# Optimization experiments

Hardware: AMD Instinct MI355X
Metric: run time of the kernel (lower is better)

## Reference

```python
import jax, jax.numpy as jnp
import numpy as np
from jax import lax

B, T, N = 4, 48, 2000
F, H, HEADS, HOR, K = 16, 64, 4, 24, 3
P = H // 2
EPS_BN = 1e-5
EPS_LN = 1e-5
NEG = -1e9


def layer_norm(x, g, b):
    mu = jnp.mean(x, axis=-1, keepdims=True)
    var = jnp.var(x, axis=-1, keepdims=True)
    return (x - mu) * jax.lax.rsqrt(var + EPS_LN) * g + b


def setup_inputs() -> dict:
    key = jax.random.key(0)
    ks = jax.random.split(key, 16)
    s = lambda k, shp, sc: jax.random.normal(k, shp, jnp.float32) * sc
    return {
        "x": s(ks[0], (B, T, N), 1.0),
        "conv_w": s(ks[1], (F, 1, K), 0.3),
        "conv_b": jnp.zeros((F,), jnp.float32),
        "bn_g": jnp.ones((F,), jnp.float32),
        "bn_b": jnp.zeros((F,), jnp.float32),
        "proj_w": s(ks[2], (H, F * T), 0.03),
        "proj_b": jnp.zeros((H,), jnp.float32),
        "ln1_g": jnp.ones((H,), jnp.float32),
        "ln1_b": jnp.zeros((H,), jnp.float32),
        "src_w": s(ks[3], (P, H), 0.1),
        "src_b": jnp.zeros((P,), jnp.float32),
        "dst_w": s(ks[4], (P, H), 0.1),
        "dst_b": jnp.zeros((P,), jnp.float32),
        "edge_scale": jnp.ones((1,), jnp.float32),
        "in_proj_w": s(ks[5], (3 * H, H), 0.1),
        "in_proj_b": jnp.zeros((3 * H,), jnp.float32),
        "out_w": s(ks[6], (H, H), 0.1),
        "out_b": jnp.zeros((H,), jnp.float32),
        "lnA_g": jnp.ones((H,), jnp.float32),
        "lnA_b": jnp.zeros((H,), jnp.float32),
        "pred_w": s(ks[7], (HOR, H), 0.1),
        "pred_b": jnp.zeros((HOR,), jnp.float32),
    }


def reference(x, conv_w, conv_b, bn_g, bn_b, proj_w, proj_b, ln1_g, ln1_b,
              src_w, src_b, dst_w, dst_b, edge_scale,
              in_proj_w, in_proj_b, out_w, out_b, lnA_g, lnA_b,
              pred_w, pred_b):
    # ---- temporal encoding: [B,T,N] -> [B*N,1,T] conv1d(same) ----
    xt = jnp.transpose(x, (0, 2, 1)).reshape(B * N, 1, T)
    h = lax.conv_general_dilated(xt, conv_w, (1,), "SAME",
                                 dimension_numbers=("NCH", "OIH", "NCH"))
    h = h + conv_b[None, :, None]
    # BatchNorm1d in eval mode (running_mean=0, running_var=1)
    h = h * (bn_g * lax.rsqrt(jnp.float32(1.0 + EPS_BN)))[None, :, None] + bn_b[None, :, None]
    h = jax.nn.relu(h)
    # ---- feature projector: flatten [F,T] -> hidden ----
    flat = h.reshape(B * N, F * T)
    z = flat @ proj_w.T + proj_b
    z = jax.nn.relu(layer_norm(z, ln1_g, ln1_b))
    node = z.reshape(B, N, H)
    # ---- dynamic graph generation ----
    src = jax.nn.leaky_relu(node @ src_w.T + src_b, 0.2)  # [B,N,P]
    dst = jax.nn.leaky_relu(node @ dst_w.T + dst_b, 0.2)
    adj = jnp.einsum("bnp,bmp->bnm", src, dst) * edge_scale[0]
    norm = jnp.maximum(jnp.linalg.norm(adj, axis=-1, keepdims=True), 1e-12)
    adj = adj / norm + jnp.eye(N, dtype=adj.dtype)[None]
    neg_mask = jnp.where(adj <= 0, jnp.float32(NEG), jnp.float32(0.0))  # [B,N,N]
    # ---- relational attention (single layer) ----
    residual = node
    qkv = node @ in_proj_w.T + in_proj_b  # [B,N,3H]
    q, k, v = jnp.split(qkv, 3, axis=-1)
    d = H // HEADS
    qh = q.reshape(B, N, HEADS, d)
    kh = k.reshape(B, N, HEADS, d)
    vh = v.reshape(B, N, HEADS, d)
    scores = jnp.einsum("bqhd,bkhd->bhqk", qh, kh) / jnp.sqrt(jnp.float32(d))
    attn = jax.nn.softmax(scores, axis=-1)
    y = jnp.einsum("bhqk,bkhd->bqhd", attn, vh).reshape(B, N, H)
    y = y @ out_w.T + out_b
    # second (adjacency-masked) attention recompute
    w2 = jnp.einsum("bnd,bmd->bnm", y, y) / jnp.sqrt(jnp.float32(H)) + neg_mask
    w2 = jax.nn.softmax(w2, axis=-1)
    y = jnp.einsum("bnm,bmd->bnd", w2, y)
    y = layer_norm(y + residual, lnA_g, lnA_b)
    # ---- horizon predictor ----
    return y @ pred_w.T + pred_b  # [B,N,HOR]
```

## Files before the change

kernel.cpp:

```cpp
#include <hip/hip_runtime.h>
#include <hip/hip_bf16.h>


#define NB 4
#define TT 48
#define NNODES 2000
#define HORZ 24
#define PART_Q 8000

#define D4(a,b) ((a).x*(b).x + (a).y*(b).y + (a).z*(b).z + (a).w*(b).w)
#define FMA4(o,p,v) { (o).x = fmaf((p),(v).x,(o).x); (o).y = fmaf((p),(v).y,(o).y); \
                      (o).z = fmaf((p),(v).z,(o).z); (o).w = fmaf((p),(v).w,(o).w); }

typedef __attribute__((ext_vector_type(8))) short short8;
typedef __attribute__((ext_vector_type(4))) float f32x4;
#define MFMA16(a,b,c) __builtin_amdgcn_mfma_f32_16x16x32_bf16((a),(b),(c),0,0,0)

__device__ __forceinline__ float wsum64(float v) {
#pragma unroll
    for (int m = 1; m < 64; m <<= 1) v += __shfl_xor(v, m, 64);
    return v;
}
__device__ __forceinline__ unsigned short f2bf(float x) {
    unsigned u = __float_as_uint(x);
    unsigned r = (u + 0x7fffu + ((u >> 16) & 1u)) >> 16;
    return (unsigned short)r;
}
__device__ __forceinline__ float bf2f(unsigned short h) {
    return __uint_as_float((unsigned)h << 16);
}

__global__ __launch_bounds__(256) void k_tr(const float* __restrict__ pw,
                                            float* __restrict__ pT) {
    int i = blockIdx.x * 256 + threadIdx.x;
    int h = i / 768, j = i - h * 768;
    pT[((j >> 2) * 64 + h) * 4 + (j & 3)] = pw[i];
}

__global__ __launch_bounds__(64) void k_enc(const float* __restrict__ x,
        const float* __restrict__ cw, const float* __restrict__ cb,
        const float* __restrict__ bg, const float* __restrict__ bb,
        const float* __restrict__ pT, const float* __restrict__ pb,
        const float* __restrict__ g1, const float* __restrict__ b1,
        float* __restrict__ node) {
    __shared__ float xs[8][52];
    __shared__ float hs[8][768];
    __shared__ float wc[16][4];
    int tid = threadIdx.x;
    int g0 = blockIdx.x * 8;

    if (tid < 16) {
        float s = bg[tid] * rsqrtf(1.0f + 1e-5f);
        wc[tid][0] = cw[tid * 3 + 0] * s;
        wc[tid][1] = cw[tid * 3 + 1] * s;
        wc[tid][2] = cw[tid * 3 + 2] * s;
        wc[tid][3] = cb[tid] * s + bb[tid];
    }
    for (int i = tid; i < 8 * TT; i += 64) {
        int m = i & 7, t = i >> 3;
        int g = g0 + m;
        int b = g / NNODES, n = g - b * NNODES;
        xs[m][t + 1] = x[(b * TT + t) * NNODES + n];
    }
    if (tid < 8) { xs[tid][0] = 0.f; xs[tid][TT + 1] = 0.f; }
    __syncthreads();

    for (int m = 0; m < 8; m++) {
        for (int j = tid; j < 16 * TT; j += 64) {
            int f = j / TT, t = j - f * TT;
            float h = wc[f][0] * xs[m][t] + wc[f][1] * xs[m][t + 1] +
                      wc[f][2] * xs[m][t + 2] + wc[f][3];
            hs[m][j] = fmaxf(h, 0.f);
        }
    }
    __syncthreads();

    float acc[8];
    float pbv = pb[tid];
#pragma unroll
    for (int m = 0; m < 8; m++) acc[m] = pbv;
    const float4* pT4v = (const float4*)pT;
    for (int jb = 0; jb < 192; ++jb) {
        float4 wv = pT4v[jb * 64 + tid];
#pragma unroll
        for (int m = 0; m < 8; m++) {
            float4 hv = *(const float4*)&hs[m][jb * 4];
            acc[m] += D4(wv, hv);
        }
    }
    float gg = g1[tid], bbv = b1[tid];
    for (int m = 0; m < 8; m++) {
        float v = acc[m];
        float sm = wsum64(v);
        float sq = wsum64(v * v);
        float mu = sm * (1.f / 64.f);
        float var = sq * (1.f / 64.f) - mu * mu;
        float z = (v - mu) * rsqrtf(var + 1e-5f) * gg + bbv;
        node[(g0 + m) * 64 + tid] = fmaxf(z, 0.f);
    }
}

__global__ __launch_bounds__(256) void k_qkv(const float* __restrict__ node,
        const float* __restrict__ ipw, const float* __restrict__ ipb,
        const float* __restrict__ sw, const float* __restrict__ sb,
        const float* __restrict__ dw, const float* __restrict__ db,
        float* __restrict__ Qb, float* __restrict__ Kb, float* __restrict__ Vb,
        float* __restrict__ Sb, float* __restrict__ Db) {
    __shared__ float nds[8][64];
    int tid = threadIdx.x;
    int g0 = blockIdx.x * 8;
    for (int i = tid; i < 8 * 64; i += 256) {
        nds[i >> 6][i & 63] = node[(size_t)g0 * 64 + i];
    }
    __syncthreads();

    int o = tid;
    const float* wrow; float bias;
    if (o < 192)      { wrow = ipw + o * 64;          bias = ipb[o]; }
    else if (o < 224) { wrow = sw + (o - 192) * 64;   bias = sb[o - 192]; }
    else              { wrow = dw + (o - 224) * 64;   bias = db[o - 224]; }

    float acc[8];
#pragma unroll
    for (int n = 0; n < 8; ++n) acc[n] = bias;

#pragma unroll
    for (int c = 0; c < 4; ++c) {
        const float4* wp = (const float4*)(wrow + c * 16);
        float4 w0 = wp[0], w1 = wp[1], w2 = wp[2], w3 = wp[3];
#pragma unroll
        for (int n = 0; n < 8; ++n) {
            const float4* nr = (const float4*)&nds[n][c * 16];
            float4 a0 = nr[0], a1 = nr[1], a2 = nr[2], a3 = nr[3];
            acc[n] += D4(a0, w0) + D4(a1, w1) + D4(a2, w2) + D4(a3, w3);
        }
    }

    if (o < 64) {
#pragma unroll
        for (int n = 0; n < 8; ++n) Qb[(size_t)(g0 + n) * 64 + o] = acc[n] * 0.25f;
    } else if (o < 128) {
        int oo = o - 64;
#pragma unroll
        for (int n = 0; n < 8; ++n) Kb[(size_t)(g0 + n) * 64 + oo] = acc[n];
    } else if (o < 192) {
        int oo = o - 128;
#pragma unroll
        for (int n = 0; n < 8; ++n) Vb[(size_t)(g0 + n) * 64 + oo] = acc[n];
    } else if (o < 224) {
        int oo = o - 192;
#pragma unroll
        for (int n = 0; n < 8; ++n) {
            float a = acc[n];
            Sb[(size_t)(g0 + n) * 32 + oo] = (a >= 0.f ? a : 0.2f * a);
        }
    } else {
        int oo = o - 224;
#pragma unroll
        for (int n = 0; n < 8; ++n) {
            float a = acc[n];
            Db[(size_t)(g0 + n) * 32 + oo] = (a >= 0.f ? a : 0.2f * a);
        }
    }
}

__global__ __launch_bounds__(256) void k_adj(const float* __restrict__ Sbuf,
        const float* __restrict__ Dbuf, const float* __restrict__ es_p,
        unsigned* __restrict__ maskT, float* __restrict__ ssqP,
        float* __restrict__ adv) {
    __shared__ float Sl[64][32];
    __shared__ float ssqW[4][64];
    int tid = threadIdx.x, bid = blockIdx.x;
    int b = bid >> 7, qt = (bid >> 2) & 31, mc = bid & 3;
    int w = tid >> 6, l = tid & 63;
    int bbase = b * NNODES;
    int qg0 = bbase + qt * 64;
    float es = es_p[0];

    for (int k = 0; k < 2; ++k) {
        int idx = tid + k * 256;
        int row = idx >> 3, cc = idx & 7;
        int qv = qt * 64 + row;
        *(float4*)&Sl[row][cc * 4] =
            *(const float4*)(Sbuf + (size_t)(bbase + min(qv, NNODES - 1)) * 32 + cc * 4);
    }
    __syncthreads();

    float ssqAcc = 0.f;
#pragma unroll
    for (int tt = 0; tt < 2; ++tt) {
        int t = w + tt * 4;
        int mb = mc * 512 + t * 64 + l;
        bool mok = mb < NNODES;
        float4 dr[8];
        const float4* dp = (const float4*)(Dbuf + (size_t)(bbase + (mok ? mb : NNODES - 1)) * 32);
#pragma unroll
        for (int j = 0; j < 8; ++j) dr[j] = dp[j];

        unsigned long long bits = 0ull;
        for (int qq = 0; qq < 64; ++qq) {
            int qv = qt * 64 + qq;
            const float4* sp = (const float4*)&Sl[qq][0];
            float a = 0.f;
#pragma unroll
            for (int j = 0; j < 8; ++j) a += D4(sp[j], dr[j]);
            a *= es;
            if (!mok) a = 0.f;
            bool diag = (mb == qv);
            if (diag && qv < NNODES) adv[qg0 + qq] = a;
            bits |= ((a > 0.f && !diag) ? 1ull : 0ull) << qq;
            float ssqq = wsum64(a * a);
            if (qq == l) ssqAcc += ssqq;
        }
        maskT[((size_t)(b * 64) + qt * 2) * 2048 + mb] = (unsigned)bits;
        maskT[((size_t)(b * 64) + qt * 2 + 1) * 2048 + mb] = (unsigned)(bits >> 32);
    }
    ssqW[w][l] = ssqAcc;
    __syncthreads();
    if (tid < 64) {
        int qv = qt * 64 + tid;
        if (qv < NNODES)
            ssqP[(size_t)mc * PART_Q + qg0 + tid] =
                ssqW[0][tid] + ssqW[1][tid] + ssqW[2][tid] + ssqW[3][tid];
    }
}

__global__ __launch_bounds__(256) void k_diag(const float* __restrict__ ssqP,
        const float* __restrict__ adv, unsigned* __restrict__ maskT) {
    int qg = blockIdx.x * 256 + threadIdx.x;
    if (qg >= PART_Q) return;
    float ss = ssqP[qg] + ssqP[PART_Q + qg] + ssqP[2 * PART_Q + qg] + ssqP[3 * PART_Q + qg];
    float norm = fmaxf(sqrtf(ss), 1e-12f);
    if (adv[qg] > -norm) {
        int b = qg / NNODES, ql = qg - b * NNODES;
        maskT[((size_t)(b * 64) + (ql >> 5)) * 2048 + ql] |= (1u << (ql & 31));
    }
}

__global__ __launch_bounds__(256, 2) void k_a1(const float* __restrict__ Qb,
        const float* __restrict__ Kb, const float* __restrict__ Vb,
        float* __restrict__ Part) {
    __shared__ float Kl[125][64];
    __shared__ float Vl[125][64];
    int tid = threadIdx.x, bid = blockIdx.x;
    int b = bid >> 7, qb = (bid >> 4) & 7, mc = bid & 15;
    int bbase = b * NNODES;
    int w = tid >> 6, l = tid & 63;
    int h = l >> 4, qs = l & 15;
    int qloc0 = qb * 256 + w * 64 + qs;

    for (int k = 0; k < 16; ++k) {
        int idx = tid + k * 256;
        if (idx < 4000) {
            int arr = idx >= 2000 ? 1 : 0;
            int e = arr ? idx - 2000 : idx;
            int r = e >> 4, cc = e & 15;
            int mb = mc * 125 + r;
            float4 v = *(const float4*)((arr ? Vb : Kb) + (size_t)(bbase + mb) * 64 + cc * 4);
            float* dst = arr ? &Vl[0][0] : &Kl[0][0];
            *(float4*)(dst + r * 64 + cc * 4) = v;
        }
    }

    float4 qf[4][4], fo[4][4];
    float sm[4];
#pragma unroll
    for (int qi = 0; qi < 4; ++qi) {
        int qrow = bbase + min(qloc0 + 16 * qi, NNODES - 1);
        const float4* qp = (const float4*)(Qb + (size_t)qrow * 64 + h * 16);
#pragma unroll
        for (int j = 0; j < 4; ++j) {
            qf[qi][j] = qp[j];
            fo[qi][j] = make_float4(0.f, 0.f, 0.f, 0.f);
        }
        sm[qi] = 0.f;
    }
    __syncthreads();

    for (int mi = 0; mi < 125; ++mi) {
        const float4* kr = (const float4*)(&Kl[mi][h * 16]);
        float4 k0 = kr[0], k1 = kr[1], k2 = kr[2], k3 = kr[3];
        float p[4];
#pragma unroll
        for (int qi = 0; qi < 4; ++qi) {
            float s = D4(qf[qi][0], k0) + D4(qf[qi][1], k1) +
                      D4(qf[qi][2], k2) + D4(qf[qi][3], k3);
            p[qi] = __expf(s);
            sm[qi] += p[qi];
        }
        const float4* vr = (const float4*)(&Vl[mi][h * 16]);
        float4 v0 = vr[0], v1 = vr[1], v2 = vr[2], v3 = vr[3];
#pragma unroll
        for (int qi = 0; qi < 4; ++qi) {
            FMA4(fo[qi][0], p[qi], v0) FMA4(fo[qi][1], p[qi], v1)
            FMA4(fo[qi][2], p[qi], v2) FMA4(fo[qi][3], p[qi], v3)
        }
    }

#pragma unroll
    for (int qi = 0; qi < 4; ++qi) {
        int qloc = qloc0 + 16 * qi;
        if (qloc < NNODES) {
            float* base = Part + (size_t)(mc * 68) * PART_Q + bbase + qloc;
#pragma unroll
            for (int j = 0; j < 4; ++j) {
                base[(size_t)(h * 16 + j * 4 + 0) * PART_Q] = fo[qi][j].x;
                base[(size_t)(h * 16 + j * 4 + 1) * PART_Q] = fo[qi][j].y;
                base[(size_t)(h * 16 + j * 4 + 2) * PART_Q] = fo[qi][j].z;
                base[(size_t)(h * 16 + j * 4 + 3) * PART_Q] = fo[qi][j].w;
            }
            base[(size_t)(64 + h) * PART_Q] = sm[qi];
        }
    }
}

__global__ __launch_bounds__(256) void k_a1m(const float* __restrict__ Part,
        const float* __restrict__ ow, const float* __restrict__ ob,
        float* __restrict__ y1) {
    __shared__ float owl[64][64];
    int tid = threadIdx.x;
    for (int i = tid; i < 4096; i += 256) ((float*)owl)[i] = ow[i];
    __syncthreads();
    int qg = blockIdx.x * 256 + tid;
    if (qg >= PART_Q) return;
    float acc[68];
#pragma unroll
    for (int k = 0; k < 68; ++k) acc[k] = 0.f;
    for (int mc = 0; mc < 16; ++mc) {
        const float* p = Part + (size_t)(mc * 68) * PART_Q + qg;
#pragma unroll
        for (int k = 0; k < 68; ++k) acc[k] += p[(size_t)k * PART_Q];
    }
#pragma unroll
    for (int e = 0; e < 64; ++e) acc[e] /= acc[64 + (e >> 4)];
    float* yo = y1 + (size_t)qg * 64;
    for (int d = 0; d < 64; d += 4) {
        float rr[4];
#pragma unroll
        for (int u = 0; u < 4; ++u) {
            float s = ob[d + u];
            const float4* wr = (const float4*)&owl[d + u][0];
#pragma unroll
            for (int e4 = 0; e4 < 16; ++e4) {
                float4 w4 = wr[e4];
                s = fmaf(acc[e4 * 4 + 0], w4.x, s);
                s = fmaf(acc[e4 * 4 + 1], w4.y, s);
                s = fmaf(acc[e4 * 4 + 2], w4.z, s);
                s = fmaf(acc[e4 * 4 + 3], w4.w, s);
            }
            rr[u] = s;
        }
        *(float4*)(yo + d) = make_float4(rr[0], rr[1], rr[2], rr[3]);
    }
}

__global__ __launch_bounds__(256, 2) void k_a2(const float* __restrict__ y1,
        const unsigned* __restrict__ maskTg, float* __restrict__ Part) {
    __shared__ unsigned short Yhi[64 * 72];
    __shared__ unsigned short Ylo[64 * 72];
    __shared__ unsigned short Yt[64 * 72];
    __shared__ unsigned short Pl[4 * 16 * 72];
    __shared__ unsigned maskTl[2 * 256];

    int tid = threadIdx.x, bid = blockIdx.x;
    int b = bid >> 8, qt = (bid >> 3) & 31, mc = bid & 7;
    int wv = tid >> 6, l = tid & 63;
    int l15 = l & 15, lg = l >> 4;
    const float* y1b = y1 + (size_t)(b * NNODES) * 64;

    for (int i = tid; i < 512; i += 256) {
        int wq = i >> 8, ml = i & 255;
        int mg = mc * 256 + ml;
        maskTl[wq * 256 + ml] =
            (mg < NNODES) ? maskTg[((size_t)(b * 64) + qt * 2 + wq) * 2048 + mg] : 0u;
    }

    int qloc_f = min(qt * 64 + wv * 16 + l15, NNODES - 1);
    const float* qrow = y1b + (size_t)qloc_f * 64;
    short8 Ahi0, Ahi1, Alo0, Alo1;
#pragma unroll
    for (int j = 0; j < 8; ++j) {
        float x0 = qrow[lg * 8 + j];
        unsigned short h0 = f2bf(x0);
        Ahi0[j] = (short)h0; Alo0[j] = (short)f2bf(x0 - bf2f(h0));
        float x1 = qrow[32 + lg * 8 + j];
        unsigned short h1 = f2bf(x1);
        Ahi1[j] = (short)h1; Alo1[j] = (short)f2bf(x1 - bf2f(h1));
    }

    f32x4 O0 = {0.f,0.f,0.f,0.f}, O1 = {0.f,0.f,0.f,0.f};
    f32x4 O2 = {0.f,0.f,0.f,0.f}, O3 = {0.f,0.f,0.f,0.f};
    float sumAcc[4] = {0.f, 0.f, 0.f, 0.f};
    int wvbase = wv * 16 * 72;
    int bitb = (wv & 1) * 16 + lg * 4;
    int mword = wv >> 1;

    for (int step = 0; step < 4; ++step) {
        int m0 = mc * 256 + step * 64;
        for (int i = tid; i < 1024; i += 256) {
            int r = i >> 4, c4 = i & 15;
            int mg = m0 + r;
            float4 v = make_float4(0.f, 0.f, 0.f, 0.f);
            if (mg < NNODES) v = *(const float4*)(y1b + (size_t)mg * 64 + c4 * 4);
            unsigned short h0 = f2bf(v.x), h1 = f2bf(v.y), h2 = f2bf(v.z), h3 = f2bf(v.w);
            ushort4 hv = {h0, h1, h2, h3};
            *(ushort4*)&Yhi[r * 72 + c4 * 4] = hv;
            ushort4 lv = {f2bf(v.x - bf2f(h0)), f2bf(v.y - bf2f(h1)),
                          f2bf(v.z - bf2f(h2)), f2bf(v.w - bf2f(h3))};
            *(ushort4*)&Ylo[r * 72 + c4 * 4] = lv;
            Yt[(c4 * 4 + 0) * 72 + r] = h0;
            Yt[(c4 * 4 + 1) * 72 + r] = h1;
            Yt[(c4 * 4 + 2) * 72 + r] = h2;
            Yt[(c4 * 4 + 3) * 72 + r] = h3;
        }
        __syncthreads();

#pragma unroll
        for (int mt = 0; mt < 4; ++mt) {
            int mrow = mt * 16 + l15;
            short8 bh0 = *(const short8*)&Yhi[mrow * 72 + lg * 8];
            short8 bh1 = *(const short8*)&Yhi[mrow * 72 + 32 + lg * 8];
            short8 bl0 = *(const short8*)&Ylo[mrow * 72 + lg * 8];
            short8 bl1 = *(const short8*)&Ylo[mrow * 72 + 32 + lg * 8];
            f32x4 S = {0.f, 0.f, 0.f, 0.f};
            S = MFMA16(Ahi0, bh0, S); S = MFMA16(Ahi1, bh1, S);
            S = MFMA16(Alo0, bh0, S); S = MFMA16(Alo1, bh1, S);
            S = MFMA16(Ahi0, bl0, S); S = MFMA16(Ahi1, bl1, S);
            unsigned mwv = maskTl[mword * 256 + step * 64 + mt * 16 + l15];
#pragma unroll
            for (int r = 0; r < 4; ++r) {
                float p = ((mwv >> (bitb + r)) & 1u) ? __expf(S[r] * 0.125f) : 0.f;
                sumAcc[r] += p;
                Pl[wvbase + (lg * 4 + r) * 72 + mt * 16 + l15] = f2bf(p);
            }
        }

#pragma unroll
        for (int ks = 0; ks < 2; ++ks) {
            short8 pf = *(const short8*)&Pl[wvbase + l15 * 72 + ks * 32 + lg * 8];
            short8 v0 = *(const short8*)&Yt[(0 * 16 + l15) * 72 + ks * 32 + lg * 8];
            O0 = MFMA16(pf, v0, O0);
            short8 v1 = *(const short8*)&Yt[(1 * 16 + l15) * 72 + ks * 32 + lg * 8];
            O1 = MFMA16(pf, v1, O1);
            short8 v2 = *(const short8*)&Yt[(2 * 16 + l15) * 72 + ks * 32 + lg * 8];
            O2 = MFMA16(pf, v2, O2);
            short8 v3 = *(const short8*)&Yt[(3 * 16 + l15) * 72 + ks * 32 + lg * 8];
            O3 = MFMA16(pf, v3, O3);
        }
        __syncthreads();
    }

#pragma unroll
    for (int r = 0; r < 4; ++r) {
        float s = sumAcc[r];
        s += __shfl_xor(s, 1, 64); s += __shfl_xor(s, 2, 64);
        s += __shfl_xor(s, 4, 64); s += __shfl_xor(s, 8, 64);
        sumAcc[r] = s;
    }
    int qrow_base = qt * 64 + wv * 16 + lg * 4;
#pragma unroll
    for (int r = 0; r < 4; ++r) {
        int qloc = qrow_base + r;
        if (qloc < NNODES) {
            float* pp = Part + ((size_t)(mc * 8192) + b * 2048 + qloc) * 72;
            pp[0 * 16 + l15] = O0[r];
            pp[1 * 16 + l15] = O1[r];
            pp[2 * 16 + l15] = O2[r];
            pp[3 * 16 + l15] = O3[r];
            if (l15 == 0) pp[64] = sumAcc[r];
        }
    }
}

__global__ __launch_bounds__(256) void k_a2m(const float* __restrict__ Part,
        const float* __restrict__ node,
        const float* __restrict__ ga, const float* __restrict__ ba,
        const float* __restrict__ pw, const float* __restrict__ pb,
        float* __restrict__ out) {
    __shared__ float pwl[24 * 64];
    __shared__ float gal[64], bal[64], pbl[24];
    int tid = threadIdx.x;
    for (int i = tid; i < 24 * 64; i += 256) pwl[i] = pw[i];
    if (tid < 64) { gal[tid] = ga[tid]; bal[tid] = ba[tid]; }
    if (tid < 24) pbl[tid] = pb[tid];
    __syncthreads();
    int t = blockIdx.x * 256 + tid;
    int b = t >> 11, ql = t & 2047;
    if (ql >= NNODES) return;
    int qg = b * NNODES + ql;

    float acc[65];
#pragma unroll
    for (int k = 0; k < 65; ++k) acc[k] = 0.f;
    for (int mc = 0; mc < 8; ++mc) {
        const float* p = Part + ((size_t)(mc * 8192) + b * 2048 + ql) * 72;
#pragma unroll
        for (int k = 0; k < 65; ++k) acc[k] += p[k];
    }
    float inv = 1.0f / acc[64];
    const float* nd = node + (size_t)qg * 64;
    float oo[64];
    float s1 = 0.f, s2 = 0.f;
#pragma unroll
    for (int d = 0; d < 64; ++d) {
        float v = acc[d] * inv + nd[d];
        oo[d] = v;
        s1 += v; s2 += v * v;
    }
    float mu = s1 * (1.f / 64.f);
    float var = s2 * (1.f / 64.f) - mu * mu;
    float rs = rsqrtf(var + 1e-5f);
#pragma unroll
    for (int d = 0; d < 64; ++d) oo[d] = (oo[d] - mu) * rs * gal[d] + bal[d];

    float* op = out + (size_t)qg * HORZ;
    for (int r = 0; r < HORZ; ++r) {
        float s = pbl[r];
        const float4* wr = (const float4*)&pwl[r * 64];
#pragma unroll
        for (int e4 = 0; e4 < 16; ++e4) {
            float4 w4 = wr[e4];
            s = fmaf(oo[e4 * 4 + 0], w4.x, s);
            s = fmaf(oo[e4 * 4 + 1], w4.y, s);
            s = fmaf(oo[e4 * 4 + 2], w4.z, s);
            s = fmaf(oo[e4 * 4 + 3], w4.w, s);
        }
        op[r] = s;
    }
}

extern "C" void kernel_launch(void* const* d_in, const int* in_sizes, int n_in,
                              void* d_out, int out_size, void* d_ws, size_t ws_size,
                              hipStream_t stream) {
    const float* x      = (const float*)d_in[0];
    const float* conv_w = (const float*)d_in[1];
    const float* conv_b = (const float*)d_in[2];
    const float* bn_g   = (const float*)d_in[3];
    const float* bn_b   = (const float*)d_in[4];
    const float* proj_w = (const float*)d_in[5];
    const float* proj_b = (const float*)d_in[6];
    const float* ln1_g  = (const float*)d_in[7];
    const float* ln1_b  = (const float*)d_in[8];
    const float* src_w  = (const float*)d_in[9];
    const float* src_b  = (const float*)d_in[10];
    const float* dst_w  = (const float*)d_in[11];
    const float* dst_b  = (const float*)d_in[12];
    const float* edge_s = (const float*)d_in[13];
    const float* ipw    = (const float*)d_in[14];
    const float* ipb    = (const float*)d_in[15];
    const float* out_w  = (const float*)d_in[16];
    const float* out_b  = (const float*)d_in[17];
    const float* lnA_g  = (const float*)d_in[18];
    const float* lnA_b  = (const float*)d_in[19];
    const float* pred_w = (const float*)d_in[20];
    const float* pred_b = (const float*)d_in[21];
    float* out = (float*)d_out;

    float* ws = (float*)d_ws;
    float*    projT = ws;
    float*    node  = projT + 49152;
    float*    y1    = node + 512000;
    float*    Qb    = y1 + 512000;
    float*    Kb    = Qb + 512000;
    float*    Vb    = Kb + 512000;
    float*    Sbuf  = Vb + 512000;
    float*    Dbuf  = Sbuf + 256000;
    unsigned* maskT = (unsigned*)(Dbuf + 256000);
    float*    ssqP  = (float*)(maskT + 524288);
    float*    adv   = ssqP + 32000;
    float*    Part  = adv + 8000;

    k_tr<<<192, 256, 0, stream>>>(proj_w, projT);
    k_enc<<<1000, 64, 0, stream>>>(x, conv_w, conv_b, bn_g, bn_b,
                                   projT, proj_b, ln1_g, ln1_b, node);
    k_qkv<<<1000, 256, 0, stream>>>(node, ipw, ipb, src_w, src_b, dst_w, dst_b,
                                    Qb, Kb, Vb, Sbuf, Dbuf);
    k_adj<<<512, 256, 0, stream>>>(Sbuf, Dbuf, edge_s, maskT, ssqP, adv);
    k_diag<<<32, 256, 0, stream>>>(ssqP, adv, maskT);
    k_a1<<<512, 256, 0, stream>>>(Qb, Kb, Vb, Part);
    k_a1m<<<32, 256, 0, stream>>>(Part, out_w, out_b, y1);
    k_a2<<<1024, 256, 0, stream>>>(y1, maskT, Part);
    k_a2m<<<32, 256, 0, stream>>>(Part, node, lnA_g, lnA_b, pred_w, pred_b, out);
}
```

Baseline: 402.8 us.

## Move first attention to bf16 MFMA with split-precision QK and repartition

Rewrites the unmasked multi-head attention kernel to use 16x16x32 bf16 MFMA instructions instead of scalar FP32 dot products. Q and K are split into hi/lo bf16 parts (three-term product) to keep the score precision near FP32, while P and V go through plain bf16 via LDS staging. The grid is repartitioned into 1024 blocks over 64-query tiles and 8 key chunks, and the partial buffer layout becomes row-major per query, with the merge kernel updated to match. The risk is bf16 rounding error in the P*V product and the extra LDS traffic for converting and transposing K/V.

```diff
diff --git a/kernel.cpp b/kernel.cpp
--- a/kernel.cpp
+++ b/kernel.cpp
@@ -9,8 +9,6 @@
 #define PART_Q 8000
 
 #define D4(a,b) ((a).x*(b).x + (a).y*(b).y + (a).z*(b).z + (a).w*(b).w)
-#define FMA4(o,p,v) { (o).x = fmaf((p),(v).x,(o).x); (o).y = fmaf((p),(v).y,(o).y); \
-                      (o).z = fmaf((p),(v).z,(o).z); (o).w = fmaf((p),(v).w,(o).w); }
 
 typedef __attribute__((ext_vector_type(8))) short short8;
 typedef __attribute__((ext_vector_type(4))) float f32x4;
@@ -240,76 +238,121 @@
 __global__ __launch_bounds__(256, 2) void k_a1(const float* __restrict__ Qb,
         const float* __restrict__ Kb, const float* __restrict__ Vb,
         float* __restrict__ Part) {
-    __shared__ float Kl[125][64];
-    __shared__ float Vl[125][64];
+    __shared__ unsigned short Khi[64 * 72];
+    __shared__ unsigned short Klo[64 * 72];
+    __shared__ unsigned short Vt[64 * 73];
+    __shared__ unsigned short Pl[4 * 16 * 72];
+
     int tid = threadIdx.x, bid = blockIdx.x;
-    int b = bid >> 7, qb = (bid >> 4) & 7, mc = bid & 15;
+    int b = bid >> 8, qt = (bid >> 3) & 31, mc = bid & 7;
     int bbase = b * NNODES;
-    int w = tid >> 6, l = tid & 63;
-    int h = l >> 4, qs = l & 15;
-    int qloc0 = qb * 256 + w * 64 + qs;
-
-    for (int k = 0; k < 16; ++k) {
-        int idx = tid + k * 256;
-        if (idx < 4000) {
-            int arr = idx >= 2000 ? 1 : 0;
-            int e = arr ? idx - 2000 : idx;
-            int r = e >> 4, cc = e & 15;
-            int mb = mc * 125 + r;
-            float4 v = *(const float4*)((arr ? Vb : Kb) + (size_t)(bbase + mb) * 64 + cc * 4);
-            float* dst = arr ? &Vl[0][0] : &Kl[0][0];
-            *(float4*)(dst + r * 64 + cc * 4) = v;
-        }
-    }
-
-    float4 qf[4][4], fo[4][4];
-    float sm[4];
-#pragma unroll
-    for (int qi = 0; qi < 4; ++qi) {
-        int qrow = bbase + min(qloc0 + 16 * qi, NNODES - 1);
-        const float4* qp = (const float4*)(Qb + (size_t)qrow * 64 + h * 16);
-#pragma unroll
-        for (int j = 0; j < 4; ++j) {
-            qf[qi][j] = qp[j];
-            fo[qi][j] = make_float4(0.f, 0.f, 0.f, 0.f);
-        }
-        sm[qi] = 0.f;
-    }
-    __syncthreads();
-
-    for (int mi = 0; mi < 125; ++mi) {
-        const float4* kr = (const float4*)(&Kl[mi][h * 16]);
-        float4 k0 = kr[0], k1 = kr[1], k2 = kr[2], k3 = kr[3];
-        float p[4];
-#pragma unroll
-        for (int qi = 0; qi < 4; ++qi) {
-            float s = D4(qf[qi][0], k0) + D4(qf[qi][1], k1) +
-                      D4(qf[qi][2], k2) + D4(qf[qi][3], k3);
-            p[qi] = __expf(s);
-            sm[qi] += p[qi];
-        }
-        const float4* vr = (const float4*)(&Vl[mi][h * 16]);
-        float4 v0 = vr[0], v1 = vr[1], v2 = vr[2], v3 = vr[3];
-#pragma unroll
-        for (int qi = 0; qi < 4; ++qi) {
-            FMA4(fo[qi][0], p[qi], v0) FMA4(fo[qi][1], p[qi], v1)
-            FMA4(fo[qi][2], p[qi], v2) FMA4(fo[qi][3], p[qi], v3)
-        }
-    }
-
-#pragma unroll
-    for (int qi = 0; qi < 4; ++qi) {
-        int qloc = qloc0 + 16 * qi;
+    int wv = tid >> 6, l = tid & 63;
+    int l15 = l & 15, lg = l >> 4;
+    bool hiSel = (lg < 2);
+    int dof = (lg & 1) * 8;
+
+    int qloc_f = min(qt * 64 + wv * 16 + l15, NNODES - 1);
+    const float* qrow = Qb + (size_t)(bbase + qloc_f) * 64;
+    short8 A1[4], A2[4];
+#pragma unroll
+    for (int h = 0; h < 4; ++h) {
+#pragma unroll
+        for (int j = 0; j < 8; ++j) {
+            float v = qrow[h * 16 + dof + j];
+            unsigned short hv = f2bf(v);
+            unsigned short lv = f2bf(v - bf2f(hv));
+            A1[h][j] = (short)(hiSel ? hv : lv);
+            A2[h][j] = (short)(hiSel ? hv : 0);
+        }
+    }
+
+    f32x4 O[4];
+#pragma unroll
+    for (int h = 0; h < 4; ++h) O[h] = (f32x4){0.f, 0.f, 0.f, 0.f};
+    float sumAcc[16];
+#pragma unroll
+    for (int i = 0; i < 16; ++i) sumAcc[i] = 0.f;
+    short8 zz = {0, 0, 0, 0, 0, 0, 0, 0};
+    int plb = wv * 1152;
+
+    for (int step = 0; step < 4; ++step) {
+        int m0 = mc * 256 + step * 64;
+        for (int i = tid; i < 1024; i += 256) {
+            int r = i >> 4, c4 = i & 15;
+            int mg = m0 + r;
+            float4 v = make_float4(0.f, 0.f, 0.f, 0.f);
+            if (mg < NNODES) v = *(const float4*)(Kb + (size_t)(bbase + mg) * 64 + c4 * 4);
+            unsigned short h0 = f2bf(v.x), h1 = f2bf(v.y), h2 = f2bf(v.z), h3 = f2bf(v.w);
+            ushort4 hv = {h0, h1, h2, h3};
+            *(ushort4*)&Khi[r * 72 + c4 * 4] = hv;
+            ushort4 lv = {f2bf(v.x - bf2f(h0)), f2bf(v.y - bf2f(h1)),
+                          f2bf(v.z - bf2f(h2)), f2bf(v.w - bf2f(h3))};
+            *(ushort4*)&Klo[r * 72 + c4 * 4] = lv;
+        }
+        for (int i = tid; i < 1024; i += 256) {
+            int r = i >> 4, c4 = i & 15;
+            int mg = m0 + r;
+            float4 v = make_float4(0.f, 0.f, 0.f, 0.f);
+            if (mg < NNODES) v = *(const float4*)(Vb + (size_t)(bbase + mg) * 64 + c4 * 4);
+            Vt[(c4 * 4 + 0) * 73 + r] = f2bf(v.x);
+            Vt[(c4 * 4 + 1) * 73 + r] = f2bf(v.y);
+            Vt[(c4 * 4 + 2) * 73 + r] = f2bf(v.z);
+            Vt[(c4 * 4 + 3) * 73 + r] = f2bf(v.w);
+        }
+        __syncthreads();
+
+#pragma unroll
+        for (int h = 0; h < 4; ++h) {
+#pragma unroll
+            for (int mt = 0; mt < 4; ++mt) {
+                int mrow = mt * 16 + l15;
+                short8 b1 = *(const short8*)&Khi[mrow * 72 + h * 16 + dof];
+                short8 b2 = *(const short8*)&Klo[mrow * 72 + h * 16 + dof];
+                if (!hiSel) b2 = zz;
+                f32x4 S = {0.f, 0.f, 0.f, 0.f};
+                S = MFMA16(A1[h], b1, S);
+                S = MFMA16(A2[h], b2, S);
+                int mglob = m0 + mrow;
+#pragma unroll
+                for (int r = 0; r < 4; ++r) {
+                    float p = (mglob < NNODES) ? __expf(S[r]) : 0.f;
+                    sumAcc[h * 4 + r] += p;
+                    Pl[plb + (lg * 4 + r) * 72 + mrow] = f2bf(p);
+                }
+            }
+#pragma unroll
+            for (int ks = 0; ks < 2; ++ks) {
+                short8 pf = *(const short8*)&Pl[plb + l15 * 72 + ks * 32 + lg * 8];
+                short8 vf = *(const short8*)&Vt[(h * 16 + l15) * 73 + ks * 32 + lg * 8];
+                O[h] = MFMA16(pf, vf, O[h]);
+            }
+        }
+        __syncthreads();
+    }
+
+#pragma unroll
+    for (int i = 0; i < 16; ++i) {
+        float s = sumAcc[i];
+        s += __shfl_xor(s, 1, 64); s += __shfl_xor(s, 2, 64);
+        s += __shfl_xor(s, 4, 64); s += __shfl_xor(s, 8, 64);
+        sumAcc[i] = s;
+    }
+    int qrow0 = qt * 64 + wv * 16 + lg * 4;
+#pragma unroll
+    for (int r = 0; r < 4; ++r) {
+        int qloc = qrow0 + r;
         if (qloc < NNODES) {
-            float* base = Part + (size_t)(mc * 68) * PART_Q + bbase + qloc;
-#pragma unroll
-            for (int j = 0; j < 4; ++j) {
-                base[(size_t)(h * 16 + j * 4 + 0) * PART_Q] = fo[qi][j].x;
-                base[(size_t)(h * 16 + j * 4 + 1) * PART_Q] = fo[qi][j].y;
-                base[(size_t)(h * 16 + j * 4 + 2) * PART_Q] = fo[qi][j].z;
-                base[(size_t)(h * 16 + j * 4 + 3) * PART_Q] = fo[qi][j].w;
+            float* pp = Part + ((size_t)(mc * 8192) + b * 2048 + qloc) * 72;
+            pp[0 * 16 + l15] = O[0][r];
+            pp[1 * 16 + l15] = O[1][r];
+            pp[2 * 16 + l15] = O[2][r];
+            pp[3 * 16 + l15] = O[3][r];
+            if (l15 == 0) {
+                pp[64] = sumAcc[0 * 4 + r];
+                pp[65] = sumAcc[1 * 4 + r];
+                pp[66] = sumAcc[2 * 4 + r];
+                pp[67] = sumAcc[3 * 4 + r];
             }
-            base[(size_t)(64 + h) * PART_Q] = sm[qi];
         }
     }
 }
@@ -321,19 +364,21 @@
     int tid = threadIdx.x;
     for (int i = tid; i < 4096; i += 256) ((float*)owl)[i] = ow[i];
     __syncthreads();
-    int qg = blockIdx.x * 256 + tid;
-    if (qg >= PART_Q) return;
+    int t = blockIdx.x * 256 + tid;
+    int b = t >> 11, ql = t & 2047;
+    if (ql >= NNODES) return;
+
     float acc[68];
 #pragma unroll
     for (int k = 0; k < 68; ++k) acc[k] = 0.f;
-    for (int mc = 0; mc < 16; ++mc) {
-        const float* p = Part + (size_t)(mc * 68) * PART_Q + qg;
-#pragma unroll
-        for (int k = 0; k < 68; ++k) acc[k] += p[(size_t)k * PART_Q];
+    for (int mc = 0; mc < 8; ++mc) {
+        const float* p = Part + ((size_t)(mc * 8192) + b * 2048 + ql) * 72;
+#pragma unroll
+        for (int k = 0; k < 68; ++k) acc[k] += p[k];
     }
 #pragma unroll
     for (int e = 0; e < 64; ++e) acc[e] /= acc[64 + (e >> 4)];
-    float* yo = y1 + (size_t)qg * 64;
+    float* yo = y1 + (size_t)(b * NNODES + ql) * 64;
     for (int d = 0; d < 64; d += 4) {
         float rr[4];
 #pragma unroll
@@ -577,7 +622,7 @@
                                     Qb, Kb, Vb, Sbuf, Dbuf);
     k_adj<<<512, 256, 0, stream>>>(Sbuf, Dbuf, edge_s, maskT, ssqP, adv);
     k_diag<<<32, 256, 0, stream>>>(ssqP, adv, maskT);
-    k_a1<<<512, 256, 0, stream>>>(Qb, Kb, Vb, Part);
+    k_a1<<<1024, 256, 0, stream>>>(Qb, Kb, Vb, Part);
     k_a1m<<<32, 256, 0, stream>>>(Part, out_w, out_b, y1);
     k_a2<<<1024, 256, 0, stream>>>(y1, maskT, Part);
     k_a2m<<<32, 256, 0, stream>>>(Part, node, lnA_g, lnA_b, pred_w, pred_b, out);
```

Result: faster. 368.6 us (-8.5%).
